# Performance work log

Hardware: AMD Instinct MI355X
Metric: run time of the kernel (lower is better)

The kernel has to match this reference:

```python
import jax, jax.numpy as jnp
import numpy as np

B, N, H = 64, 128, 6
V, NPOS, NPOST = 30000, 60, 160
ED, PD = 300, 30
RH = 300            # rnn_hidden == hidden_dim (mem_dim)
D = 2 * RH          # d_model = 600
DK = D // H         # 100
NLAYERS = 2
POL = 3
IN_DIM = ED + 2 * PD  # 360
SQRT_DK = np.float32(np.sqrt(DK))


def _lstm_dir(x, Wih, Whh, b):
    # x: [B,T,I]; torch gate order i,f,g,o
    xg = jnp.einsum('bti,gi->btg', x, Wih) + b
    h0 = jnp.zeros((x.shape[0], Whh.shape[1]), x.dtype)

    def step(carry, xt):
        h, c = carry
        g = xt + h @ Whh.T
        i, f, gg, o = jnp.split(g, 4, axis=-1)
        c = jax.nn.sigmoid(f) * c + jax.nn.sigmoid(i) * jnp.tanh(gg)
        h = jax.nn.sigmoid(o) * jnp.tanh(c)
        return (h, c), h

    _, hs = jax.lax.scan(step, (h0, h0), jnp.swapaxes(xg, 0, 1))
    return jnp.swapaxes(hs, 0, 1)


def _forward(floats, ints):
    (emb_w, pos_w, post_w, Wih_f, Whh_f, b_f, Wih_b, Whh_b, b_b,
     Wq, bq, Wk, bk, Wd, bd, weight_m, bias_m, Ww, bw, Wx, bx,
     Wxx, bxx, Wc, bc, mask, short) = floats
    tok, pos_ids, post_ids = ints
    # embedding concat [B,N,360]
    embs = jnp.concatenate([emb_w[tok], pos_w[pos_ids], post_w[post_ids]], axis=-1)
    # bidirectional LSTM (all lengths full -> reverse == flip)
    fwd = _lstm_dir(embs, Wih_f, Whh_f, b_f)
    bwd = _lstm_dir(embs[:, ::-1], Wih_b, Whh_b, b_b)[:, ::-1]
    g_in = jnp.concatenate([fwd, bwd], axis=-1)       # [B,N,D]
    asp_wn = mask.sum(axis=1, keepdims=True)          # [B,1]
    aspect = (g_in * mask[..., None]).sum(axis=1) / asp_wn  # [B,D]
    # aspect-biased multi-head attention adjacency
    q = (g_in @ Wq.T + bq).reshape(B, N, H, DK).transpose(0, 2, 1, 3)
    k = (g_in @ Wk.T + bk).reshape(B, N, H, DK).transpose(0, 2, 1, 3)
    scores = jnp.einsum('bhnd,bhmd->bhnm', q, k) / SQRT_DK
    a = aspect @ Wd.T + bd                            # [B,DK] (same across heads)
    aw = jnp.einsum('bd,hde->bhe', a, weight_m)       # aspect @ weight_m
    asc = jnp.tanh(jnp.einsum('bhe,bhme->bhm', aw, k) + bias_m[0])[:, :, None, :]
    scores = scores + asc
    src = (tok != 0)[:, None, None, :]
    scores = jnp.where(src, scores, -1e9) + short
    adj = jax.nn.softmax(scores, axis=-1)             # [B,H,N,N]
    # iterative dense GCN aggregation + edge (adjacency) update
    g = g_in
    for _ in range(NLAYERS):
        Ax = jnp.einsum('bhnm,bmd->bnd', adj, g) / H  # per-head matmul, mean over heads
        g = jax.nn.selu(Ax @ Ww.T + bw)               # [B,N,D]
        # edge = cat([adj_perm, node1, node2]) @ Wx.T + bx, computed without
        # materializing the [B,N,N,H+2D] concat: split Wx along its input dim.
        ea = jnp.einsum('bhnm,kh->bnmk', adj, Wx[:, :H])
        gn1 = g @ Wx[:, H:H + D].T                    # node1[b,i,j] = g[b,j]
        gn2 = g @ Wx[:, H + D:].T                     # node2[b,i,j] = g[b,i]
        edge = ea + gn1[:, None, :, :] + gn2[:, :, None, :] + bx
        adj = edge.transpose(0, 3, 1, 2)              # back to [B,H,N,N]
    hnode = jax.nn.relu(g @ Wxx.T + bxx)              # [B,N,RH]
    pooled = (hnode * mask[..., None]).sum(axis=1) / asp_wn
    return pooled @ Wc.T + bc                         # logits [B,POL]


def setup_inputs() -> dict:
    key = jax.random.key(0)
    ks = iter(jax.random.split(key, 48))

    def rn(shape, s=0.1):
        return jax.random.normal(next(ks), shape, dtype=jnp.float32) * s

    inp = {}
    inp['tok'] = jax.random.randint(next(ks), (B, N), 1, V)
    inp['asp'] = jax.random.randint(next(ks), (B, N), 1, V)
    inp['pos_ids'] = jax.random.randint(next(ks), (B, N), 1, NPOS)
    inp['head'] = jax.random.randint(next(ks), (B, N), 0, N)
    inp['deprel'] = jax.random.randint(next(ks), (B, N), 0, 50)
    inp['post_ids'] = jax.random.randint(next(ks), (B, N), 1, NPOST)
    inp['mask'] = jnp.ones((B, N), jnp.float32)
    inp['l'] = jnp.full((B,), N, dtype=jnp.int32)
    inp['short'] = rn((B, 1, N, N), 0.1)
    inp['emb_w'] = rn((V, ED))
    inp['pos_w'] = rn((NPOS, PD))
    inp['post_w'] = rn((NPOST, PD))
    inp['Wih_f'] = rn((4 * RH, IN_DIM)); inp['Whh_f'] = rn((4 * RH, RH)); inp['b_f'] = rn((4 * RH,))
    inp['Wih_b'] = rn((4 * RH, IN_DIM)); inp['Whh_b'] = rn((4 * RH, RH)); inp['b_b'] = rn((4 * RH,))
    inp['Wq'] = rn((D, D)); inp['bq'] = rn((D,))
    inp['Wk'] = rn((D, D)); inp['bk'] = rn((D,))
    inp['Wd'] = rn((DK, D)); inp['bd'] = rn((DK,))
    inp['weight_m'] = rn((H, DK, DK)); inp['bias_m'] = rn((1,))
    inp['Ww'] = rn((D, D)); inp['bw'] = rn((D,))
    inp['Wx'] = rn((H, H + 2 * D)); inp['bx'] = rn((H,))
    inp['Wxx'] = rn((RH, D)); inp['bxx'] = rn((RH,))
    inp['Wc'] = rn((POL, RH)); inp['bc'] = rn((POL,))
    return inp


def reference(tok, asp, pos_ids, head, deprel, post_ids, mask, l, short,
              emb_w, pos_w, post_w, Wih_f, Whh_f, b_f, Wih_b, Whh_b, b_b,
              Wq, bq, Wk, bk, Wd, bd, weight_m, bias_m, Ww, bw, Wx, bx,
              Wxx, bxx, Wc, bc):
    floats = (emb_w, pos_w, post_w, Wih_f, Whh_f, b_f, Wih_b, Whh_b, b_b,
              Wq, bq, Wk, bk, Wd, bd, weight_m, bias_m, Ww, bw, Wx, bx,
              Wxx, bxx, Wc, bc, mask, short)
    return _forward(floats, (tok, pos_ids, post_ids))
```

## Files before the change

### kernel.cpp

```cpp
#include <hip/hip_runtime.h>
#include <math.h>

#define BB    64
#define NN_   128
#define NH    6
#define DM    600
#define RHID  300
#define DKH   100
#define INDIM 360
#define G4    1200
#define WXROW 1206
#define DMP   608
#define INP   384
#define QKL   1536

#define S_CL  25
#define NSU   12
#define NSR   48
#define KPAD  320
#define HSLOT (BB*KPAD)
#define DSTR  (129*HSLOT)

#define OFF_GINB   0ull
#define OFF_ASPECT 2490368ull
#define OFF_ASCB   2573568ull
#define OFF_W1SUM  2622720ull
#define OFF_W2SUM  2623360ull
#define OFF_SWX    2624000ull
#define OFF_SBX    2624016ull
#define OFF_SGI    2624032ull
#define OFF_WHS    2640416ull
#define OFF_WQKP   3688992ull
#define OFF_BQK    4155936ull
#define OFF_WWP    4157472ull
#define OFF_WXXP   4339872ull
#define OFF_WIHPF  4431072ull
#define OFF_WIHPB  4661472ull
#define OFF_BPF    4891872ull
#define OFF_BPB    4893072ull
#define OFF_WTB    4894272ull
#define OFF_EMBS   5278272ull
#define ARENA      6851136ull
#define OFF_XGF    (ARENA)
#define OFF_XGB    (ARENA + 4915200ull)
#define OFF_HIST   (ARENA + 9830400ull)
#define OFF_FLAGS  (ARENA + 12472320ull)
#define OFF_QKH    (ARENA)
#define OFF_ADJ    (ARENA + 6291456ull)
#define OFF_ADJS   (ARENA + 16121856ull)
#define OFF_GINT   (ARENA + 16646144ull)
#define OFF_W12    (ARENA + 19136512ull)
#define OFF_WDM    (ARENA + 19137152ull)
#define OFF_BDM    (ARENA + 19497152ull)
#define OFF_AXB    (ARENA)
#define OFF_G1B    (ARENA + 2490368ull)
#define OFF_G1T    (OFF_GINT)
#define OFF_AX2B   (ARENA + 4980736ull)
#define OFF_G2B    (ARENA + 7471104ull)
#define OFF_HNB    (ARENA + 9961472ull)

typedef __bf16 bf16x8 __attribute__((ext_vector_type(8)));
typedef __bf16 bf16x4 __attribute__((ext_vector_type(4)));
typedef __bf16 bf16x2 __attribute__((ext_vector_type(2)));
typedef float  f32x4  __attribute__((ext_vector_type(4)));

__device__ __forceinline__ float sigm(float x){ return 1.f/(1.f+__expf(-x)); }
__device__ __forceinline__ float selu_f(float x){
  const float sc=1.0507009873554805f, al=1.6732632423543772f;
  return x>0.f ? sc*x : sc*al*(__expf(x)-1.f);
}
__device__ __forceinline__ bf16x8 bzero8(){
  bf16x8 z;
#pragma unroll
  for (int j=0;j<8;++j) z[j]=(__bf16)0.f;
  return z;
}

__global__ __launch_bounds__(384) void embed_k(
    const int* __restrict__ tok, const int* __restrict__ pos_ids, const int* __restrict__ post_ids,
    const float* __restrict__ emb_w, const float* __restrict__ pos_w, const float* __restrict__ post_w,
    __bf16* __restrict__ embs)
{
  int bn = blockIdx.x, t = threadIdx.x;
  float v = 0.f;
  if      (t < 300) v = emb_w [(size_t)tok     [bn]*300 + t];
  else if (t < 330) v = pos_w [(size_t)pos_ids [bn]*30  + (t-300)];
  else if (t < 360) v = post_w[(size_t)post_ids[bn]*30  + (t-330)];
  embs[(size_t)bn*INP + t] = (__bf16)v;
}

__global__ __launch_bounds__(640) void consts_k(
    const float* __restrict__ Wx, const float* __restrict__ bx,
    float* __restrict__ w1sum, float* __restrict__ w2sum,
    float* __restrict__ swx, float* __restrict__ sbx, __bf16* __restrict__ w12)
{
  int t = threadIdx.x;
  if (t < DM){
    float s1=0.f, s2=0.f;
    for (int k=0;k<NH;++k){ s1 += Wx[k*WXROW + NH + t]; s2 += Wx[k*WXROW + NH + DM + t]; }
    w1sum[t]=s1; w2sum[t]=s2;
    w12[t]=(__bf16)s1; w12[DMP+t]=(__bf16)s2;
  } else if (t < DM+NH){
    int h=t-DM; float s=0.f;
    for (int k=0;k<NH;++k) s += Wx[k*WXROW + h];
    swx[h]=s;
  } else if (t == DM+NH){
    float s=0.f; for (int k=0;k<NH;++k) s += bx[k];
    sbx[0]=s;
  }
  if (t >= DM && t < DMP){ w12[t]=(__bf16)0.f; w12[DMP+t]=(__bf16)0.f; }
}

__global__ __launch_bounds__(128) void wdm_k(
    const float* __restrict__ Wd, const float* __restrict__ bd, const float* __restrict__ wm,
    float* __restrict__ WdM, float* __restrict__ bdM)
{
  int D = blockIdx.x, h = blockIdx.y, e = threadIdx.x;
  if (e >= DKH) return;
  float s = 0.f;
  for (int d=0; d<DKH; ++d)
    s += Wd[d*DM + D] * wm[(h*DKH+d)*DKH + e];
  WdM[((size_t)h*DM + D)*DKH + e] = s;
  if (D == 0){
    float sb = 0.f;
    for (int d=0; d<DKH; ++d) sb += bd[d]*wm[(h*DKH+d)*DKH + e];
    bdM[h*DKH + e] = sb;
  }
}

__global__ __launch_bounds__(256) void wihp_k(
    const float* __restrict__ WihF, const float* __restrict__ bF,
    const float* __restrict__ WihB, const float* __restrict__ bB,
    __bf16* __restrict__ wpF, float* __restrict__ bpF,
    __bf16* __restrict__ wpB, float* __restrict__ bpB)
{
  const float* Wih = blockIdx.y ? WihB : WihF;
  const float* b   = blockIdx.y ? bB   : bF;
  __bf16* wp       = blockIdx.y ? wpB  : wpF;
  float* bp        = blockIdx.y ? bpB  : bpF;
  int idx = blockIdx.x*256 + threadIdx.x;
  if (idx < G4*INP){
    int p = idx / INP, k = idx - p*INP;
    int srow = (p&3)*RHID + (p>>2);
    wp[idx] = (k<INDIM) ? (__bf16)Wih[(size_t)srow*INDIM + k] : (__bf16)0.f;
  } else if (idx < G4*INP + G4){
    int p = idx - G4*INP;
    bp[p] = b[(p&3)*RHID + (p>>2)];
  }
}

__global__ __launch_bounds__(256) void wqkhp_k(
    const float* __restrict__ Wq, const float* __restrict__ bq,
    const float* __restrict__ Wk, const float* __restrict__ bk,
    __bf16* __restrict__ wp, float* __restrict__ bp)
{
  int idx = blockIdx.x*256 + threadIdx.x;
  if (idx < QKL*DMP){
    int n = idx / DMP, k = idx - n*DMP;
    int nl = (n < 768) ? n : n - 768;
    int h = nl >> 7, e = nl & 127;
    float v = 0.f;
    if (k < DM && e < DKH)
      v = (n < 768) ? Wq[(size_t)(h*DKH+e)*DM + k] : Wk[(size_t)(h*DKH+e)*DM + k];
    wp[idx] = (__bf16)v;
  } else if (idx < QKL*DMP + QKL){
    int n = idx - QKL*DMP;
    int nl = (n < 768) ? n : n - 768;
    int h = nl >> 7, e = nl & 127;
    bp[n] = (e < DKH) ? ((n < 768) ? bq[h*DKH+e] : bk[h*DKH+e]) : 0.f;
  }
}

__global__ __launch_bounds__(256) void wpk_k(
    const float* __restrict__ W, __bf16* __restrict__ wp, int nrows, int ksrc, int kp)
{
  int idx = blockIdx.x*256 + threadIdx.x;
  if (idx >= nrows*kp) return;
  int n = idx / kp, k = idx - n*kp;
  wp[idx] = (k < ksrc) ? (__bf16)W[(size_t)n*ksrc + k] : (__bf16)0.f;
}

__global__ __launch_bounds__(256) void whhp_k(
    const float* __restrict__ WhhF, const float* __restrict__ WhhB, __bf16* __restrict__ outW)
{
  const float* Whh = blockIdx.y ? WhhB : WhhF;
  __bf16* wp = outW + (size_t)blockIdx.y * G4 * KPAD;
  int idx = blockIdx.x*256 + threadIdx.x;
  if (idx >= G4*KPAD) return;
  int p = idx / KPAD, k = idx - p*KPAD;
  wp[idx] = (k < RHID) ? (__bf16)Whh[((size_t)((p&3)*RHID + (p>>2)))*RHID + k] : (__bf16)0.f;
}

__global__ __launch_bounds__(256) void init_k(float* __restrict__ ws)
{
  int idx = blockIdx.x*256 + threadIdx.x;
  if (idx < 10240)       ws[OFF_HIST + idx] = 0.f;
  else if (idx < 20480)  ws[OFF_HIST + 1320960ull + (idx-10240)] = 0.f;
  else if (idx < 22528)  ws[OFF_FLAGS + (idx-20480)] = 0.f;
}

template<int KT, int ACT, int OBF>
__global__ __launch_bounds__(256) void wgemm_k(
    const __bf16* __restrict__ A, const __bf16* __restrict__ B,
    const float* __restrict__ bias, void* __restrict__ Cout,
    int Nn, int Npad, int ldc,
    long long sA, long long sB, long long sC)
{
  const int tid = threadIdx.x, lane = tid & 63, wave = tid >> 6;
  const int fn = lane & 15, fq = lane >> 4;
  const int K = KT*32;
  const __bf16* Ab = A + (size_t)blockIdx.z * (size_t)sA;
  const __bf16* Bb = B + (size_t)blockIdx.z * (size_t)sB;
  float*  Cf = (float*) Cout + (size_t)blockIdx.z * (size_t)sC;
  __bf16* Ch = (__bf16*)Cout + (size_t)blockIdx.z * (size_t)sC;

  const int m0 = (blockIdx.x*4 + wave)*16;

  bf16x8 Af[KT];
#pragma unroll
  for (int kt=0; kt<KT; ++kt)
    Af[kt] = *(const bf16x8*)(Ab + (size_t)(m0 + fn)*K + kt*32 + fq*8);

  for (int n0 = blockIdx.y*16; n0 < Nn; n0 += 16*gridDim.y){
    const int gn = n0 + fn;
    const int gnc = (gn < Nn) ? gn : 0;
    f32x4 acc0 = {0.f,0.f,0.f,0.f};
    f32x4 acc1 = {0.f,0.f,0.f,0.f};
#pragma unroll
    for (int kt=0; kt<KT; ++kt){
      bf16x8 Bf = *(const bf16x8*)(Bb + (size_t)gnc*K + kt*32 + fq*8);
      if (gn >= Nn) Bf = bzero8();
      if (kt & 1) acc1 = __builtin_amdgcn_mfma_f32_16x16x32_bf16(Af[kt], Bf, acc1, 0, 0, 0);
      else        acc0 = __builtin_amdgcn_mfma_f32_16x16x32_bf16(Af[kt], Bf, acc0, 0, 0, 0);
    }
    float bv = (bias && gn < Nn) ? bias[gn] : 0.f;
#pragma unroll
    for (int r=0; r<4; ++r){
      int gm = m0 + fq*4 + r;
      float v = acc0[r] + acc1[r] + bv;
      if (ACT==1) v = selu_f(v);
      else if (ACT==2) v = fmaxf(v, 0.f);
      if (gn < Nn){
        if (OBF) Ch[(size_t)gm*ldc + gn] = (__bf16)v;
        else     Cf[(size_t)gm*ldc + gn] = v;
      } else if (gn < Npad){
        if (OBF) Ch[(size_t)gm*ldc + gn] = (__bf16)0.f;
        else     Cf[(size_t)gm*ldc + gn] = 0.f;
      }
    }
  }
}

__global__ __launch_bounds__(256) void tr_k(
    const __bf16* __restrict__ in, __bf16* __restrict__ out)
{
  const int b = blockIdx.z, m0 = blockIdx.y*64, d0 = blockIdx.x*64;
  const int tid = threadIdx.x;
  __shared__ __align__(16) __bf16 T[64][72];
  const __bf16* ib = in + (size_t)b*NN_*DMP;
  __bf16* ob = out + (size_t)b*DMP*NN_;
#pragma unroll
  for (int r=0;r<2;++r){
    int idx = tid + 256*r;
    int mi = idx>>3, ch = idx&7;
    int d = d0 + ch*8;
    bf16x8 v = bzero8();
    if (d < DMP) v = *(const bf16x8*)(ib + (size_t)(m0+mi)*DMP + d);
    *(bf16x8*)&T[mi][ch*8] = v;
  }
  __syncthreads();
#pragma unroll
  for (int r=0;r<2;++r){
    int idx = tid + 256*r;
    int di = idx>>3, mch = idx&7;
    int d = d0 + di;
    if (d >= DMP) continue;
    bf16x8 v;
#pragma unroll
    for (int j=0;j<8;++j) v[j] = T[mch*8+j][di];
    *(bf16x8*)(ob + (size_t)d*NN_ + m0 + mch*8) = v;
  }
}

__global__ __launch_bounds__(256, 1) void lstm_mfma_k(
    const __bf16* __restrict__ xgf, const __bf16* __restrict__ xgb,
    const __bf16* __restrict__ wtb,
    __bf16* hist, int* flags)
{
  const int blk = blockIdx.x;
  const int dir = blk / S_CL, sl = blk - dir*S_CL;
  const int tid = threadIdx.x, lane = tid & 63, wave = tid >> 6;
  const int p0 = sl * NSR;
  const __bf16* xg = dir ? xgb : xgf;
  const __bf16* W = wtb + (size_t)dir * G4 * KPAD;
  __bf16* hb = hist + (size_t)dir * DSTR;

  __shared__ __align__(16) float accS[NSR][68];

  const int fn = lane & 15;
  const int fk = (lane >> 4) * 8;
  const int m0 = wave * 16;

  bf16x8 Bf[3][10];
#pragma unroll
  for (int nt = 0; nt < 3; ++nt)
#pragma unroll
    for (int kt = 0; kt < 10; ++kt)
      Bf[nt][kt] = *(const bf16x8*)(W + (size_t)(p0 + nt*16 + fn)*KPAD + kt*32 + fk);

  const int b_ep = tid / 3;
  const int q_ep = tid - b_ep*3;
  const int u0 = q_ep*4;
  const bool ep = (tid < 192);
  float cst[4] = {0.f,0.f,0.f,0.f};
  const __bf16* xp = xg + ((size_t)b_ep*NN_)*G4 + p0 + u0*4;

  for (int s = 0; s < NN_; ++s){
    const int n_t = dir ? (NN_-1-s) : s;
    const __bf16* hbr = hb + (size_t)s*HSLOT;
    __bf16*       hbw = hb + (size_t)(s+1)*HSLOT;

    bf16x8 xv0, xv1;
    if (ep){
      xv0 = *(const bf16x8*)(xp + (size_t)n_t*G4);
      xv1 = *(const bf16x8*)(xp + (size_t)n_t*G4 + 8);
    }

    bf16x8 Af[10];
#pragma unroll
    for (int kt = 0; kt < 10; ++kt){
      const unsigned long long* hp =
          (const unsigned long long*)(hbr + (size_t)(m0 + fn)*KPAD + kt*32 + fk);
      union { unsigned long long u[2]; bf16x8 v; } cv;
      cv.u[0] = __hip_atomic_load(hp,   __ATOMIC_RELAXED, __HIP_MEMORY_SCOPE_SYSTEM);
      cv.u[1] = __hip_atomic_load(hp+1, __ATOMIC_RELAXED, __HIP_MEMORY_SCOPE_SYSTEM);
      Af[kt] = cv.v;
    }

    f32x4 acc[3] = { {0.f,0.f,0.f,0.f}, {0.f,0.f,0.f,0.f}, {0.f,0.f,0.f,0.f} };
#pragma unroll
    for (int kt = 0; kt < 10; ++kt)
#pragma unroll
      for (int nt = 0; nt < 3; ++nt)
        acc[nt] = __builtin_amdgcn_mfma_f32_16x16x32_bf16(Af[kt], Bf[nt][kt], acc[nt], 0, 0, 0);

#pragma unroll
    for (int nt = 0; nt < 3; ++nt)
      *(f32x4*)&accS[nt*16 + fn][m0 + (lane>>4)*4] = acc[nt];
    __syncthreads();

    if (ep){
      union { unsigned long long u; __bf16 h[4]; } pk;
      float xgv[16];
#pragma unroll
      for (int j=0;j<8;++j){ xgv[j]=(float)xv0[j]; xgv[8+j]=(float)xv1[j]; }
#pragma unroll
      for (int du = 0; du < 4; ++du){
        int u = u0 + du;
        float p_i = accS[u*4+0][b_ep] + xgv[du*4+0];
        float p_f = accS[u*4+1][b_ep] + xgv[du*4+1];
        float p_g = accS[u*4+2][b_ep] + xgv[du*4+2];
        float p_o = accS[u*4+3][b_ep] + xgv[du*4+3];
        float ig = sigm(p_i), fg = sigm(p_f), gg = tanhf(p_g), og = sigm(p_o);
        float c = fg*cst[du] + ig*gg; cst[du] = c;
        pk.h[du] = (__bf16)(og * tanhf(c));
      }
      __hip_atomic_store(
          (unsigned long long*)(hbw + (size_t)b_ep*KPAD + sl*NSU + u0),
          pk.u, __ATOMIC_RELAXED, __HIP_MEMORY_SCOPE_SYSTEM);
    }
    __syncthreads();
    if (tid == 0)
      __hip_atomic_store(&flags[(dir*S_CL + sl)*32], s+1, __ATOMIC_RELAXED, __HIP_MEMORY_SCOPE_SYSTEM);
    if (wave == 0 && lane < S_CL){
      int* fp = &flags[(dir*S_CL + lane)*32];
      while (__hip_atomic_load(fp, __ATOMIC_RELAXED, __HIP_MEMORY_SCOPE_SYSTEM) < s+1) { }
    }
    __syncthreads();
  }
}

__global__ __launch_bounds__(320) void reshape_k(
    const __bf16* __restrict__ hist, __bf16* __restrict__ ginb)
{
  int row = blockIdx.x;
  int b = row >> 7, n = row & 127;
  int t = threadIdx.x;
  if (t < 150){
    int u = 2*t;
    bf16x2 v = *(const bf16x2*)(hist + (size_t)(n+1)*HSLOT + (size_t)b*KPAD + u);
    *(bf16x2*)(ginb + (size_t)row*DMP + u) = v;
  } else if (t >= 160 && t < 310){
    int u = 2*(t-160);
    bf16x2 v = *(const bf16x2*)(hist + (size_t)DSTR + (size_t)(NN_-n)*HSLOT + (size_t)b*KPAD + u);
    *(bf16x2*)(ginb + (size_t)row*DMP + RHID + u) = v;
  } else if (t >= 312 && t < 316){
    int c = DM + 2*(t-312);
    bf16x2 z; z[0]=(__bf16)0.f; z[1]=(__bf16)0.f;
    *(bf16x2*)(ginb + (size_t)row*DMP + c) = z;
  }
}

__global__ __launch_bounds__(320) void aspect_k(
    const __bf16* __restrict__ ginb, const float* __restrict__ mask, float* __restrict__ aspect)
{
  int b = blockIdx.x, t = threadIdx.x;
  int col = blockIdx.y*300 + t;
  __shared__ float msk[NN_];
  __shared__ float wn;
  if (t < NN_) msk[t] = mask[b*NN_+t];
  __syncthreads();
  if (t==0){ float s=0.f; for (int n=0;n<NN_;++n) s+=msk[n]; wn=s; }
  __syncthreads();
  if (t < 300){
    float s=0.f;
    for (int n=0;n<NN_;++n) s += (float)ginb[((size_t)(b*NN_+n))*DMP + col]*msk[n];
    aspect[b*DM+col] = s/wn;
  }
}

__global__ __launch_bounds__(128) void ascf_k(
    const float* __restrict__ aspect, const float* __restrict__ WdM, const float* __restrict__ bdM,
    const __bf16* __restrict__ qkh, const float* __restrict__ bias_m, float* __restrict__ asc)
{
  int b = blockIdx.x, h = blockIdx.y, t = threadIdx.x;
  __shared__ __align__(16) float asp[DM];
  __shared__ __align__(16) float awl[DKH];
  for (int i = t; i < DM; i += 128) asp[i] = aspect[b*DM + i];
  __syncthreads();
  if (t < DKH){
    const float* wrow = WdM + (size_t)h*DM*DKH + t;
    float s0=0.f,s1=0.f,s2=0.f,s3=0.f;
    for (int D=0; D<DM; D+=4){
      s0 += asp[D+0]*wrow[(size_t)(D+0)*DKH];
      s1 += asp[D+1]*wrow[(size_t)(D+1)*DKH];
      s2 += asp[D+2]*wrow[(size_t)(D+2)*DKH];
      s3 += asp[D+3]*wrow[(size_t)(D+3)*DKH];
    }
    awl[t] = s0+s1+s2+s3 + bdM[h*DKH + t];
  }
  __syncthreads();
  const __bf16* kr = qkh + (size_t)(b*NN_ + t)*QKL + 768 + h*128;
  float s=0.f;
#pragma unroll
  for (int e=0;e<DKH;e+=2){
    bf16x2 kv = *(const bf16x2*)(kr + e);
    s += awl[e]*(float)kv[0] + awl[e+1]*(float)kv[1];
  }
  asc[(b*NH+h)*NN_ + t] = tanhf(s + bias_m[0]);
}

__global__ __launch_bounds__(256) void attn2_k(
    const __bf16* __restrict__ qkh, const float* __restrict__ asc,
    const float* __restrict__ shortm, const int* __restrict__ tok,
    __bf16* __restrict__ adj)
{
  const int bh = blockIdx.x, b = bh / NH, h = bh - b*NH;
  const int tid = threadIdx.x, lane = tid & 63, wave = tid >> 6;
  const int fn = lane & 15, fq = lane >> 4;
  const __bf16* qb = qkh + (size_t)(b*NN_)*QKL + h*128;
  const __bf16* kb = qkh + (size_t)(b*NN_)*QKL + 768 + h*128;

  bf16x8 Af[2][4];
#pragma unroll
  for (int t=0;t<2;++t){
    int m0 = t*64 + wave*16;
#pragma unroll
    for (int kt=0;kt<4;++kt)
      Af[t][kt] = *(const bf16x8*)(qb + (size_t)(m0+fn)*QKL + kt*32 + fq*8);
  }

  f32x4 acc[2][8];
#pragma unroll
  for (int t=0;t<2;++t)
#pragma unroll
    for (int j=0;j<8;++j) acc[t][j] = (f32x4){0.f,0.f,0.f,0.f};

#pragma unroll
  for (int j=0;j<8;++j){
    bf16x8 Bf[4];
#pragma unroll
    for (int kt=0;kt<4;++kt)
      Bf[kt] = *(const bf16x8*)(kb + (size_t)(j*16+fn)*QKL + kt*32 + fq*8);
#pragma unroll
    for (int t=0;t<2;++t)
#pragma unroll
      for (int kt=0;kt<4;++kt)
        acc[t][j] = __builtin_amdgcn_mfma_f32_16x16x32_bf16(Af[t][kt], Bf[kt], acc[t][j], 0,0,0);
  }

  float ascv[8]; int msk[8];
#pragma unroll
  for (int j=0;j<8;++j){
    int c = j*16 + fn;
    ascv[j] = asc[(b*NH+h)*NN_ + c];
    msk [j] = tok[b*NN_ + c];
  }

#pragma unroll
  for (int t=0;t<2;++t){
#pragma unroll
    for (int r=0;r<4;++r){
      int m = t*64 + wave*16 + fq*4 + r;
      float sv[8];
#pragma unroll
      for (int j=0;j<8;++j){
        int c = j*16 + fn;
        float s = acc[t][j][r]*0.1f + ascv[j];
        if (msk[j]==0) s = -1e9f;
        s += shortm[((size_t)(b*NN_+m))*NN_ + c];
        sv[j]=s;
      }
      float mx = sv[0];
#pragma unroll
      for (int j=1;j<8;++j) mx = fmaxf(mx, sv[j]);
#pragma unroll
      for (int o=1;o<16;o<<=1) mx = fmaxf(mx, __shfl_xor(mx, o, 64));
      float sum = 0.f, ev[8];
#pragma unroll
      for (int j=0;j<8;++j){ ev[j]=__expf(sv[j]-mx); sum+=ev[j]; }
#pragma unroll
      for (int o=1;o<16;o<<=1) sum += __shfl_xor(sum, o, 64);
      float inv = 1.f/sum;
#pragma unroll
      for (int j=0;j<8;++j)
        adj[(((size_t)(b*NH+h))*NN_ + m)*NN_ + j*16 + fn] = (__bf16)(ev[j]*inv);
    }
  }
}

__global__ __launch_bounds__(256) void adjsum_k(
    const __bf16* __restrict__ adj, const float* __restrict__ swx,
    __bf16* __restrict__ adjs, float* __restrict__ whs)
{
  int idx = blockIdx.x*256 + threadIdx.x;
  int b = idx >> 14, rem = idx & 16383;
  float s=0.f, w=0.f;
  for (int h=0;h<NH;++h){
    float v = (float)adj[(((size_t)b*NH+h)<<14) + rem];
    s += v; w += v*swx[h];
  }
  adjs[idx] = (__bf16)(s*(1.f/NH));
  whs [idx] = w*(1.f/NH);
}

__global__ __launch_bounds__(256) void adjsum2_k(
    const float* __restrict__ whs, const float* __restrict__ sgi,
    const float* __restrict__ sbx, __bf16* __restrict__ adjs)
{
  int idx = blockIdx.x*256 + threadIdx.x;
  int b = idx >> 14, rem = idx & 16383;
  int i = rem >> 7, j = rem & 127;
  adjs[idx] = (__bf16)(whs[idx] + (sgi[(b*NN_+j)*2] + sgi[(b*NN_+i)*2+1] + sbx[0])*(1.f/NH));
}

__global__ __launch_bounds__(320) void pooled_k(
    const float* __restrict__ hn, const float* __restrict__ mask,
    const float* __restrict__ Wc, const float* __restrict__ bc, float* __restrict__ out)
{
  int b=blockIdx.x, t=threadIdx.x;
  __shared__ float msk[NN_];
  __shared__ float pl[RHID];
  __shared__ float wn;
  if (t<NN_) msk[t]=mask[b*NN_+t];
  __syncthreads();
  if (t==0){ float s=0.f; for (int n=0;n<NN_;++n) s+=msk[n]; wn=s; }
  __syncthreads();
  if (t<RHID){
    float s=0.f;
    for (int n=0;n<NN_;++n) s += hn[((size_t)(b*NN_+n))*RHID+t]*msk[n];
    pl[t]=s/wn;
  }
  __syncthreads();
  if (t<3){
    float s=bc[t];
    for (int d=0;d<RHID;++d) s += pl[d]*Wc[t*RHID+d];
    out[b*3+t]=s;
  }
}

extern "C" void kernel_launch(void* const* d_in, const int* in_sizes, int n_in,
                              void* d_out, int out_size, void* d_ws, size_t ws_size,
                              hipStream_t stream)
{
  (void)in_sizes; (void)n_in; (void)out_size; (void)ws_size;
  const int*   tok      = (const int*)  d_in[0];
  const int*   pos_ids  = (const int*)  d_in[2];
  const int*   post_ids = (const int*)  d_in[5];
  const float* mask     = (const float*)d_in[6];
  const float* shortm   = (const float*)d_in[8];
  const float* emb_w    = (const float*)d_in[9];
  const float* pos_w    = (const float*)d_in[10];
  const float* post_w   = (const float*)d_in[11];
  const float* Wih_f    = (const float*)d_in[12];
  const float* Whh_f    = (const float*)d_in[13];
  const float* b_f      = (const float*)d_in[14];
  const float* Wih_b    = (const float*)d_in[15];
  const float* Whh_b    = (const float*)d_in[16];
  const float* b_b      = (const float*)d_in[17];
  const float* Wq       = (const float*)d_in[18];
  const float* bq       = (const float*)d_in[19];
  const float* Wk       = (const float*)d_in[20];
  const float* bk       = (const float*)d_in[21];
  const float* Wd       = (const float*)d_in[22];
  const float* bd       = (const float*)d_in[23];
  const float* weight_m = (const float*)d_in[24];
  const float* bias_m   = (const float*)d_in[25];
  const float* Ww       = (const float*)d_in[26];
  const float* bw       = (const float*)d_in[27];
  const float* Wx       = (const float*)d_in[28];
  const float* bx       = (const float*)d_in[29];
  const float* Wxx      = (const float*)d_in[30];
  const float* bxx      = (const float*)d_in[31];
  const float* Wc       = (const float*)d_in[32];
  const float* bc       = (const float*)d_in[33];

  float* ws  = (float*)d_ws;
  float* out = (float*)d_out;

  __bf16* ginb  = (__bf16*)(ws + OFF_GINB);
  float* aspect = ws + OFF_ASPECT;
  float* ascb   = ws + OFF_ASCB;
  float* w1sum  = ws + OFF_W1SUM;
  float* w2sum  = ws + OFF_W2SUM;
  float* swx    = ws + OFF_SWX;
  float* sbx    = ws + OFF_SBX;
  float* sgi    = ws + OFF_SGI;
  float* whs    = ws + OFF_WHS;
  __bf16* wqkp  = (__bf16*)(ws + OFF_WQKP);
  float* bqk    = ws + OFF_BQK;
  __bf16* wwp   = (__bf16*)(ws + OFF_WWP);
  __bf16* wxxp  = (__bf16*)(ws + OFF_WXXP);
  __bf16* wihpF = (__bf16*)(ws + OFF_WIHPF);
  __bf16* wihpB = (__bf16*)(ws + OFF_WIHPB);
  float* bpF    = ws + OFF_BPF;
  float* bpB    = ws + OFF_BPB;
  __bf16* wtb   = (__bf16*)(ws + OFF_WTB);
  __bf16* embs  = (__bf16*)(ws + OFF_EMBS);
  __bf16* xgf   = (__bf16*)(ws + OFF_XGF);
  __bf16* xgb   = (__bf16*)(ws + OFF_XGB);
  __bf16* hist  = (__bf16*)(ws + OFF_HIST);
  int*   flags  = (int*)(ws + OFF_FLAGS);
  __bf16* qkh   = (__bf16*)(ws + OFF_QKH);
  __bf16* adjb  = (__bf16*)(ws + OFF_ADJ);
  __bf16* adjs  = (__bf16*)(ws + OFF_ADJS);
  __bf16* gint  = (__bf16*)(ws + OFF_GINT);
  __bf16* w12   = (__bf16*)(ws + OFF_W12);
  float* wdm    = ws + OFF_WDM;
  float* bdm    = ws + OFF_BDM;
  __bf16* axb   = (__bf16*)(ws + OFF_AXB);
  __bf16* g1b   = (__bf16*)(ws + OFF_G1B);
  __bf16* g1t   = (__bf16*)(ws + OFF_G1T);
  __bf16* ax2b  = (__bf16*)(ws + OFF_AX2B);
  __bf16* g2b   = (__bf16*)(ws + OFF_G2B);
  float* hnb    = ws + OFF_HNB;

  embed_k<<<dim3(BB*NN_),384,0,stream>>>(tok,pos_ids,post_ids,emb_w,pos_w,post_w,embs);
  consts_k<<<1,640,0,stream>>>(Wx,bx,w1sum,w2sum,swx,sbx,w12);
  wdm_k<<<dim3(DM,NH),128,0,stream>>>(Wd,bd,weight_m,wdm,bdm);
  wihp_k<<<dim3((G4*INP+G4+255)/256,2),256,0,stream>>>(Wih_f,b_f,Wih_b,b_b,wihpF,bpF,wihpB,bpB);
  wqkhp_k<<<dim3((QKL*DMP+QKL+255)/256),256,0,stream>>>(Wq,bq,Wk,bk,wqkp,bqk);
  wpk_k<<<dim3((DM*DMP+255)/256),256,0,stream>>>(Ww,wwp,DM,DM,DMP);
  wpk_k<<<dim3((RHID*DMP+255)/256),256,0,stream>>>(Wxx,wxxp,RHID,DM,DMP);
  whhp_k<<<dim3((G4*KPAD+255)/256,2),256,0,stream>>>(Whh_f,Whh_b,wtb);
  init_k<<<dim3((22528+255)/256),256,0,stream>>>(ws);
  wgemm_k<12,0,1><<<dim3(128,8,1),256,0,stream>>>(embs,wihpF,bpF,xgf, G4,G4,G4, 0,0,0);
  wgemm_k<12,0,1><<<dim3(128,8,1),256,0,stream>>>(embs,wihpB,bpB,xgb, G4,G4,G4, 0,0,0);
  lstm_mfma_k<<<dim3(2*S_CL),256,0,stream>>>(xgf,xgb,wtb,hist,flags);
  reshape_k<<<dim3(BB*NN_),320,0,stream>>>(hist,ginb);
  wgemm_k<19,0,1><<<dim3(128,8,1),256,0,stream>>>(ginb,wqkp,bqk,qkh, QKL,QKL,QKL, 0,0,0);
  aspect_k<<<dim3(BB,2),320,0,stream>>>(ginb,mask,aspect);
  ascf_k<<<dim3(BB,NH),128,0,stream>>>(aspect,wdm,bdm,qkh,bias_m,ascb);
  attn2_k<<<dim3(BB*NH),256,0,stream>>>(qkh,ascb,shortm,tok,adjb);
  adjsum_k<<<4096,256,0,stream>>>(adjb,swx,adjs,whs);
  tr_k<<<dim3(10,2,BB),256,0,stream>>>(ginb,gint);
  wgemm_k<4,0,1><<<dim3(2,4,BB),256,0,stream>>>(adjs,gint,nullptr,axb, DM,DMP,DMP, 16384,(long long)DMP*NN_,(long long)NN_*DMP);
  wgemm_k<19,1,1><<<dim3(128,8,1),256,0,stream>>>(axb,wwp,bw,g1b, DM,DMP,DMP, 0,0,0);
  wgemm_k<19,0,0><<<dim3(128,1,1),256,0,stream>>>(g1b,w12,nullptr,sgi, 2,2,2, 0,0,0);
  adjsum2_k<<<4096,256,0,stream>>>(whs,sgi,sbx,adjs);
  tr_k<<<dim3(10,2,BB),256,0,stream>>>(g1b,g1t);
  wgemm_k<4,0,1><<<dim3(2,4,BB),256,0,stream>>>(adjs,g1t,nullptr,ax2b, DM,DMP,DMP, 16384,(long long)DMP*NN_,(long long)NN_*DMP);
  wgemm_k<19,1,1><<<dim3(128,8,1),256,0,stream>>>(ax2b,wwp,bw,g2b, DM,DMP,DMP, 0,0,0);
  wgemm_k<19,2,0><<<dim3(128,4,1),256,0,stream>>>(g2b,wxxp,bxx,hnb, RHID,RHID,RHID, 0,0,0);
  pooled_k<<<BB,320,0,stream>>>(hnb,mask,Wc,bc,out);
}
```

Baseline: 1.284 ms.

## Merge weight-packing kernels, fuse both LSTM input GEMMs, split attention blocks

Collapses the four weight-packing kernels and the workspace-init kernel into one pack_k launch. The forward and backward LSTM input projections now run as a single GEMM into an interleaved buffer of width 2400, and the LSTM kernel indexes it by direction. The QK projection GEMM gets more blocks along y, and attn2_k is split into two half-row blocks per (batch, head) pair to raise parallelism. The aim is to cut launch overhead and improve occupancy. The cost is a wider xg row stride, which may reduce locality in the LSTM's per-step loads.

```diff
diff --git a/kernel.cpp b/kernel.cpp
--- a/kernel.cpp
+++ b/kernel.cpp
@@ -13,6 +13,7 @@
 #define DMP   608
 #define INP   384
 #define QKL   1536
+#define XGW   2400
 
 #define S_CL  25
 #define NSU   12
@@ -34,15 +35,12 @@
 #define OFF_BQK    4155936ull
 #define OFF_WWP    4157472ull
 #define OFF_WXXP   4339872ull
-#define OFF_WIHPF  4431072ull
-#define OFF_WIHPB  4661472ull
-#define OFF_BPF    4891872ull
-#define OFF_BPB    4893072ull
+#define OFF_WIHP   4431072ull
+#define OFF_BP     4891872ull
 #define OFF_WTB    4894272ull
 #define OFF_EMBS   5278272ull
 #define ARENA      6851136ull
-#define OFF_XGF    (ARENA)
-#define OFF_XGB    (ARENA + 4915200ull)
+#define OFF_XG     (ARENA)
 #define OFF_HIST   (ARENA + 9830400ull)
 #define OFF_FLAGS  (ARENA + 12472320ull)
 #define OFF_QKH    (ARENA)
@@ -59,6 +57,13 @@
 #define OFF_G2B    (ARENA + 7471104ull)
 #define OFF_HNB    (ARENA + 9961472ull)
 
+#define PK0 (XGW*INP + XGW)
+#define PK1 (PK0 + QKL*DMP + QKL)
+#define PK2 (PK1 + DM*DMP)
+#define PK3 (PK2 + RHID*DMP)
+#define PK4 (PK3 + 2*G4*KPAD)
+#define PK5 (PK4 + 22528)
+
 typedef __bf16 bf16x8 __attribute__((ext_vector_type(8)));
 typedef __bf16 bf16x4 __attribute__((ext_vector_type(4)));
 typedef __bf16 bf16x2 __attribute__((ext_vector_type(2)));
@@ -128,75 +133,68 @@
   }
 }
 
-__global__ __launch_bounds__(256) void wihp_k(
-    const float* __restrict__ WihF, const float* __restrict__ bF,
-    const float* __restrict__ WihB, const float* __restrict__ bB,
-    __bf16* __restrict__ wpF, float* __restrict__ bpF,
-    __bf16* __restrict__ wpB, float* __restrict__ bpB)
-{
-  const float* Wih = blockIdx.y ? WihB : WihF;
-  const float* b   = blockIdx.y ? bB   : bF;
-  __bf16* wp       = blockIdx.y ? wpB  : wpF;
-  float* bp        = blockIdx.y ? bpB  : bpF;
-  int idx = blockIdx.x*256 + threadIdx.x;
-  if (idx < G4*INP){
-    int p = idx / INP, k = idx - p*INP;
-    int srow = (p&3)*RHID + (p>>2);
-    wp[idx] = (k<INDIM) ? (__bf16)Wih[(size_t)srow*INDIM + k] : (__bf16)0.f;
-  } else if (idx < G4*INP + G4){
-    int p = idx - G4*INP;
-    bp[p] = b[(p&3)*RHID + (p>>2)];
-  }
-}
-
-__global__ __launch_bounds__(256) void wqkhp_k(
+__global__ __launch_bounds__(256) void pack_k(
+    const float* __restrict__ Wih_f, const float* __restrict__ b_f,
+    const float* __restrict__ Wih_b, const float* __restrict__ b_b,
     const float* __restrict__ Wq, const float* __restrict__ bq,
     const float* __restrict__ Wk, const float* __restrict__ bk,
-    __bf16* __restrict__ wp, float* __restrict__ bp)
+    const float* __restrict__ Ww, const float* __restrict__ Wxx,
+    const float* __restrict__ Whh_f, const float* __restrict__ Whh_b,
+    __bf16* __restrict__ wihp, float* __restrict__ bp,
+    __bf16* __restrict__ wqkp, float* __restrict__ bqk,
+    __bf16* __restrict__ wwp, __bf16* __restrict__ wxxp,
+    __bf16* __restrict__ wtb, float* __restrict__ ws)
 {
   int idx = blockIdx.x*256 + threadIdx.x;
-  if (idx < QKL*DMP){
-    int n = idx / DMP, k = idx - n*DMP;
-    int nl = (n < 768) ? n : n - 768;
-    int h = nl >> 7, e = nl & 127;
-    float v = 0.f;
-    if (k < DM && e < DKH)
-      v = (n < 768) ? Wq[(size_t)(h*DKH+e)*DM + k] : Wk[(size_t)(h*DKH+e)*DM + k];
-    wp[idx] = (__bf16)v;
-  } else if (idx < QKL*DMP + QKL){
-    int n = idx - QKL*DMP;
-    int nl = (n < 768) ? n : n - 768;
-    int h = nl >> 7, e = nl & 127;
-    bp[n] = (e < DKH) ? ((n < 768) ? bq[h*DKH+e] : bk[h*DKH+e]) : 0.f;
-  }
-}
-
-__global__ __launch_bounds__(256) void wpk_k(
-    const float* __restrict__ W, __bf16* __restrict__ wp, int nrows, int ksrc, int kp)
-{
-  int idx = blockIdx.x*256 + threadIdx.x;
-  if (idx >= nrows*kp) return;
-  int n = idx / kp, k = idx - n*kp;
-  wp[idx] = (k < ksrc) ? (__bf16)W[(size_t)n*ksrc + k] : (__bf16)0.f;
-}
-
-__global__ __launch_bounds__(256) void whhp_k(
-    const float* __restrict__ WhhF, const float* __restrict__ WhhB, __bf16* __restrict__ outW)
-{
-  const float* Whh = blockIdx.y ? WhhB : WhhF;
-  __bf16* wp = outW + (size_t)blockIdx.y * G4 * KPAD;
-  int idx = blockIdx.x*256 + threadIdx.x;
-  if (idx >= G4*KPAD) return;
-  int p = idx / KPAD, k = idx - p*KPAD;
-  wp[idx] = (k < RHID) ? (__bf16)Whh[((size_t)((p&3)*RHID + (p>>2)))*RHID + k] : (__bf16)0.f;
-}
-
-__global__ __launch_bounds__(256) void init_k(float* __restrict__ ws)
-{
-  int idx = blockIdx.x*256 + threadIdx.x;
-  if (idx < 10240)       ws[OFF_HIST + idx] = 0.f;
-  else if (idx < 20480)  ws[OFF_HIST + 1320960ull + (idx-10240)] = 0.f;
-  else if (idx < 22528)  ws[OFF_FLAGS + (idx-20480)] = 0.f;
+  if (idx < PK0){
+    if (idx < XGW*INP){
+      int r = idx / INP, k = idx - r*INP;
+      int dir = r >= G4; int p = r - dir*G4;
+      const float* W = dir ? Wih_b : Wih_f;
+      int srow = (p&3)*RHID + (p>>2);
+      wihp[idx] = (k<INDIM) ? (__bf16)W[(size_t)srow*INDIM + k] : (__bf16)0.f;
+    } else {
+      int n = idx - XGW*INP;
+      int dir = n >= G4; int p = n - dir*G4;
+      const float* b = dir ? b_b : b_f;
+      bp[n] = b[(p&3)*RHID + (p>>2)];
+    }
+  } else if (idx < PK1){
+    int id = idx - PK0;
+    if (id < QKL*DMP){
+      int n = id / DMP, k = id - n*DMP;
+      int nl = (n < 768) ? n : n - 768;
+      int h = nl >> 7, e = nl & 127;
+      float v = 0.f;
+      if (k < DM && e < DKH)
+        v = (n < 768) ? Wq[(size_t)(h*DKH+e)*DM + k] : Wk[(size_t)(h*DKH+e)*DM + k];
+      wqkp[id] = (__bf16)v;
+    } else {
+      int n = id - QKL*DMP;
+      int nl = (n < 768) ? n : n - 768;
+      int h = nl >> 7, e = nl & 127;
+      bqk[n] = (e < DKH) ? ((n < 768) ? bq[h*DKH+e] : bk[h*DKH+e]) : 0.f;
+    }
+  } else if (idx < PK2){
+    int id = idx - PK1;
+    int n = id / DMP, k = id - n*DMP;
+    wwp[id] = (k < DM) ? (__bf16)Ww[(size_t)n*DM + k] : (__bf16)0.f;
+  } else if (idx < PK3){
+    int id = idx - PK2;
+    int n = id / DMP, k = id - n*DMP;
+    wxxp[id] = (k < DM) ? (__bf16)Wxx[(size_t)n*DM + k] : (__bf16)0.f;
+  } else if (idx < PK4){
+    int id = idx - PK3;
+    int dir = id >= G4*KPAD; int id2 = id - dir*G4*KPAD;
+    int p = id2 / KPAD, k = id2 - p*KPAD;
+    const float* Whh = dir ? Whh_b : Whh_f;
+    wtb[id] = (k < RHID) ? (__bf16)Whh[((size_t)((p&3)*RHID + (p>>2)))*RHID + k] : (__bf16)0.f;
+  } else if (idx < PK5){
+    int id = idx - PK4;
+    if (id < 10240)      ws[OFF_HIST + id] = 0.f;
+    else if (id < 20480) ws[OFF_HIST + 1320960ull + (id-10240)] = 0.f;
+    else                 ws[OFF_FLAGS + (id-20480)] = 0.f;
+  }
 }
 
 template<int KT, int ACT, int OBF>
@@ -283,7 +281,7 @@
 }
 
 __global__ __launch_bounds__(256, 1) void lstm_mfma_k(
-    const __bf16* __restrict__ xgf, const __bf16* __restrict__ xgb,
+    const __bf16* __restrict__ xg,
     const __bf16* __restrict__ wtb,
     __bf16* hist, int* flags)
 {
@@ -291,7 +289,6 @@
   const int dir = blk / S_CL, sl = blk - dir*S_CL;
   const int tid = threadIdx.x, lane = tid & 63, wave = tid >> 6;
   const int p0 = sl * NSR;
-  const __bf16* xg = dir ? xgb : xgf;
   const __bf16* W = wtb + (size_t)dir * G4 * KPAD;
   __bf16* hb = hist + (size_t)dir * DSTR;
 
@@ -313,7 +310,7 @@
   const int u0 = q_ep*4;
   const bool ep = (tid < 192);
   float cst[4] = {0.f,0.f,0.f,0.f};
-  const __bf16* xp = xg + ((size_t)b_ep*NN_)*G4 + p0 + u0*4;
+  const __bf16* xp = xg + (size_t)b_ep*NN_*XGW + dir*G4 + p0 + u0*4;
 
   for (int s = 0; s < NN_; ++s){
     const int n_t = dir ? (NN_-1-s) : s;
@@ -322,8 +319,8 @@
 
     bf16x8 xv0, xv1;
     if (ep){
-      xv0 = *(const bf16x8*)(xp + (size_t)n_t*G4);
-      xv1 = *(const bf16x8*)(xp + (size_t)n_t*G4 + 8);
+      xv0 = *(const bf16x8*)(xp + (size_t)n_t*XGW);
+      xv1 = *(const bf16x8*)(xp + (size_t)n_t*XGW + 8);
     }
 
     bf16x8 Af[10];
@@ -455,26 +452,23 @@
     const float* __restrict__ shortm, const int* __restrict__ tok,
     __bf16* __restrict__ adj)
 {
-  const int bh = blockIdx.x, b = bh / NH, h = bh - b*NH;
+  const int bx = blockIdx.x;
+  const int bh = bx >> 1, half = bx & 1;
+  const int b = bh / NH, h = bh - b*NH;
   const int tid = threadIdx.x, lane = tid & 63, wave = tid >> 6;
   const int fn = lane & 15, fq = lane >> 4;
   const __bf16* qb = qkh + (size_t)(b*NN_)*QKL + h*128;
   const __bf16* kb = qkh + (size_t)(b*NN_)*QKL + 768 + h*128;
 
-  bf16x8 Af[2][4];
-#pragma unroll
-  for (int t=0;t<2;++t){
-    int m0 = t*64 + wave*16;
-#pragma unroll
-    for (int kt=0;kt<4;++kt)
-      Af[t][kt] = *(const bf16x8*)(qb + (size_t)(m0+fn)*QKL + kt*32 + fq*8);
-  }
-
-  f32x4 acc[2][8];
-#pragma unroll
-  for (int t=0;t<2;++t)
-#pragma unroll
-    for (int j=0;j<8;++j) acc[t][j] = (f32x4){0.f,0.f,0.f,0.f};
+  const int m0 = half*64 + wave*16;
+  bf16x8 Af[4];
+#pragma unroll
+  for (int kt=0;kt<4;++kt)
+    Af[kt] = *(const bf16x8*)(qb + (size_t)(m0+fn)*QKL + kt*32 + fq*8);
+
+  f32x4 acc[8];
+#pragma unroll
+  for (int j=0;j<8;++j) acc[j] = (f32x4){0.f,0.f,0.f,0.f};
 
 #pragma unroll
   for (int j=0;j<8;++j){
@@ -483,10 +477,8 @@
     for (int kt=0;kt<4;++kt)
       Bf[kt] = *(const bf16x8*)(kb + (size_t)(j*16+fn)*QKL + kt*32 + fq*8);
 #pragma unroll
-    for (int t=0;t<2;++t)
-#pragma unroll
-      for (int kt=0;kt<4;++kt)
-        acc[t][j] = __builtin_amdgcn_mfma_f32_16x16x32_bf16(Af[t][kt], Bf[kt], acc[t][j], 0,0,0);
+    for (int kt=0;kt<4;++kt)
+      acc[j] = __builtin_amdgcn_mfma_f32_16x16x32_bf16(Af[kt], Bf[kt], acc[j], 0,0,0);
   }
 
   float ascv[8]; int msk[8];
@@ -498,34 +490,31 @@
   }
 
 #pragma unroll
-  for (int t=0;t<2;++t){
-#pragma unroll
-    for (int r=0;r<4;++r){
-      int m = t*64 + wave*16 + fq*4 + r;
-      float sv[8];
-#pragma unroll
-      for (int j=0;j<8;++j){
-        int c = j*16 + fn;
-        float s = acc[t][j][r]*0.1f + ascv[j];
-        if (msk[j]==0) s = -1e9f;
-        s += shortm[((size_t)(b*NN_+m))*NN_ + c];
-        sv[j]=s;
-      }
-      float mx = sv[0];
-#pragma unroll
-      for (int j=1;j<8;++j) mx = fmaxf(mx, sv[j]);
-#pragma unroll
-      for (int o=1;o<16;o<<=1) mx = fmaxf(mx, __shfl_xor(mx, o, 64));
-      float sum = 0.f, ev[8];
-#pragma unroll
-      for (int j=0;j<8;++j){ ev[j]=__expf(sv[j]-mx); sum+=ev[j]; }
-#pragma unroll
-      for (int o=1;o<16;o<<=1) sum += __shfl_xor(sum, o, 64);
-      float inv = 1.f/sum;
-#pragma unroll
-      for (int j=0;j<8;++j)
-        adj[(((size_t)(b*NH+h))*NN_ + m)*NN_ + j*16 + fn] = (__bf16)(ev[j]*inv);
-    }
+  for (int r=0;r<4;++r){
+    int m = m0 + fq*4 + r;
+    float sv[8];
+#pragma unroll
+    for (int j=0;j<8;++j){
+      int c = j*16 + fn;
+      float s = acc[j][r]*0.1f + ascv[j];
+      if (msk[j]==0) s = -1e9f;
+      s += shortm[((size_t)(b*NN_+m))*NN_ + c];
+      sv[j]=s;
+    }
+    float mx = sv[0];
+#pragma unroll
+    for (int j=1;j<8;++j) mx = fmaxf(mx, sv[j]);
+#pragma unroll
+    for (int o=1;o<16;o<<=1) mx = fmaxf(mx, __shfl_xor(mx, o, 64));
+    float sum = 0.f, ev[8];
+#pragma unroll
+    for (int j=0;j<8;++j){ ev[j]=__expf(sv[j]-mx); sum+=ev[j]; }
+#pragma unroll
+    for (int o=1;o<16;o<<=1) sum += __shfl_xor(sum, o, 64);
+    float inv = 1.f/sum;
+#pragma unroll
+    for (int j=0;j<8;++j)
+      adj[(((size_t)(b*NH+h))*NN_ + m)*NN_ + j*16 + fn] = (__bf16)(ev[j]*inv);
   }
 }
 
@@ -631,14 +620,11 @@
   float* bqk    = ws + OFF_BQK;
   __bf16* wwp   = (__bf16*)(ws + OFF_WWP);
   __bf16* wxxp  = (__bf16*)(ws + OFF_WXXP);
-  __bf16* wihpF = (__bf16*)(ws + OFF_WIHPF);
-  __bf16* wihpB = (__bf16*)(ws + OFF_WIHPB);
-  float* bpF    = ws + OFF_BPF;
-  float* bpB    = ws + OFF_BPB;
+  __bf16* wihp  = (__bf16*)(ws + OFF_WIHP);
+  float* bp     = ws + OFF_BP;
   __bf16* wtb   = (__bf16*)(ws + OFF_WTB);
   __bf16* embs  = (__bf16*)(ws + OFF_EMBS);
-  __bf16* xgf   = (__bf16*)(ws + OFF_XGF);
-  __bf16* xgb   = (__bf16*)(ws + OFF_XGB);
+  __bf16* xg    = (__bf16*)(ws + OFF_XG);
   __bf16* hist  = (__bf16*)(ws + OFF_HIST);
   int*   flags  = (int*)(ws + OFF_FLAGS);
   __bf16* qkh   = (__bf16*)(ws + OFF_QKH);
@@ -658,20 +644,15 @@
   embed_k<<<dim3(BB*NN_),384,0,stream>>>(tok,pos_ids,post_ids,emb_w,pos_w,post_w,embs);
   consts_k<<<1,640,0,stream>>>(Wx,bx,w1sum,w2sum,swx,sbx,w12);
   wdm_k<<<dim3(DM,NH),128,0,stream>>>(Wd,bd,weight_m,wdm,bdm);
-  wihp_k<<<dim3((G4*INP+G4+255)/256,2),256,0,stream>>>(Wih_f,b_f,Wih_b,b_b,wihpF,bpF,wihpB,bpB);
-  wqkhp_k<<<dim3((QKL*DMP+QKL+255)/256),256,0,stream>>>(Wq,bq,Wk,bk,wqkp,bqk);
-  wpk_k<<<dim3((DM*DMP+255)/256),256,0,stream>>>(Ww,wwp,DM,DM,DMP);
-  wpk_k<<<dim3((RHID*DMP+255)/256),256,0,stream>>>(Wxx,wxxp,RHID,DM,DMP);
-  whhp_k<<<dim3((G4*KPAD+255)/256,2),256,0,stream>>>(Whh_f,Whh_b,wtb);
-  init_k<<<dim3((22528+255)/256),256,0,stream>>>(ws);
-  wgemm_k<12,0,1><<<dim3(128,8,1),256,0,stream>>>(embs,wihpF,bpF,xgf, G4,G4,G4, 0,0,0);
-  wgemm_k<12,0,1><<<dim3(128,8,1),256,0,stream>>>(embs,wihpB,bpB,xgb, G4,G4,G4, 0,0,0);
-  lstm_mfma_k<<<dim3(2*S_CL),256,0,stream>>>(xgf,xgb,wtb,hist,flags);
+  pack_k<<<dim3((PK5+255)/256),256,0,stream>>>(Wih_f,b_f,Wih_b,b_b,Wq,bq,Wk,bk,Ww,Wxx,
+                                               Whh_f,Whh_b,wihp,bp,wqkp,bqk,wwp,wxxp,wtb,ws);
+  wgemm_k<12,0,1><<<dim3(128,8,1),256,0,stream>>>(embs,wihp,bp,xg, XGW,XGW,XGW, 0,0,0);
+  lstm_mfma_k<<<dim3(2*S_CL),256,0,stream>>>(xg,wtb,hist,flags);
   reshape_k<<<dim3(BB*NN_),320,0,stream>>>(hist,ginb);
-  wgemm_k<19,0,1><<<dim3(128,8,1),256,0,stream>>>(ginb,wqkp,bqk,qkh, QKL,QKL,QKL, 0,0,0);
+  wgemm_k<19,0,1><<<dim3(128,12,1),256,0,stream>>>(ginb,wqkp,bqk,qkh, QKL,QKL,QKL, 0,0,0);
   aspect_k<<<dim3(BB,2),320,0,stream>>>(ginb,mask,aspect);
   ascf_k<<<dim3(BB,NH),128,0,stream>>>(aspect,wdm,bdm,qkh,bias_m,ascb);
-  attn2_k<<<dim3(BB*NH),256,0,stream>>>(qkh,ascb,shortm,tok,adjb);
+  attn2_k<<<dim3(BB*NH*2),256,0,stream>>>(qkh,ascb,shortm,tok,adjb);
   adjsum_k<<<4096,256,0,stream>>>(adjb,swx,adjs,whs);
   tr_k<<<dim3(10,2,BB),256,0,stream>>>(ginb,gint);
   wgemm_k<4,0,1><<<dim3(2,4,BB),256,0,stream>>>(adjs,gint,nullptr,axb, DM,DMP,DMP, 16384,(long long)DMP*NN_,(long long)NN_*DMP);
```

Measured after the change: 1.270 ms. No clear change (-1.1%).
